# Kernel tuning notes

Hardware: AMD Instinct MI355X
Metric: run time of the kernel (lower is better)

Reference implementation:

```python
import jax, jax.numpy as jnp
import numpy as np

N, E, F, H, OUT = 50000, 500000, 128, 128, 768

def _lin(x, W, b):
    return x @ W + b

def _layernorm(x, g, b, eps=1e-5):
    mu = jnp.mean(x, axis=-1, keepdims=True)
    var = jnp.var(x, axis=-1, keepdims=True)
    return (x - mu) * jax.lax.rsqrt(var + eps) * g + b

def _edge_softmax(alpha, dst, n_nodes):
    # softmax over incoming edges per destination node, per channel
    amax = jax.ops.segment_max(alpha, dst, num_segments=n_nodes)
    ex = jnp.exp(alpha - amax[dst])
    denom = jax.ops.segment_sum(ex, dst, num_segments=n_nodes)
    return ex / denom[dst]

def setup_inputs() -> dict:
    key = jax.random.key(0)
    ks = jax.random.split(key, 24)
    def w(k, i, o):
        return (jax.random.normal(k, (i, o), jnp.float32) / np.float32(np.sqrt(i)))
    inp = {
        'kind': jax.random.normal(ks[0], (N, F), jnp.float32),
        'edge_h': jax.random.normal(ks[1], (E, F), jnp.float32),
        'src': jax.random.randint(ks[2], (E,), 0, N, jnp.int32),
        'dst': jax.random.randint(ks[3], (E,), 0, N, jnp.int32),
        'KW': w(ks[4], 2 * F, H), 'Kb': jnp.zeros((H,), jnp.float32),
        'VW': w(ks[5], 2 * F, H), 'Vb': jnp.zeros((H,), jnp.float32),
        'QW': w(ks[6], F, H), 'Qb': jnp.zeros((H,), jnp.float32),
        'WW': w(ks[7], F + H, H), 'Wb': jnp.zeros((H,), jnp.float32),
        'K2W': w(ks[8], 3 * F, H), 'K2b': jnp.zeros((H,), jnp.float32),
        'V2W': w(ks[9], 3 * F, H), 'V2b': jnp.zeros((H,), jnp.float32),
        'Q2W': w(ks[10], 2 * F, H), 'Q2b': jnp.zeros((H,), jnp.float32),
        'W2W': w(ks[11], 2 * F + H, OUT), 'W2b': jnp.zeros((OUT,), jnp.float32),
        'ln1_g': jnp.ones((H,), jnp.float32), 'ln1_b': jnp.zeros((H,), jnp.float32),
        'ln2_g': jnp.ones((OUT,), jnp.float32), 'ln2_b': jnp.zeros((OUT,), jnp.float32),
        'gate_w': w(ks[12], OUT, 1), 'gate_b': jnp.zeros((1,), jnp.float32),
    }
    return inp

def reference(kind, edge_h, src, dst, KW, Kb, VW, Vb, QW, Qb, WW, Wb,
              K2W, K2b, V2W, V2b, Q2W, Q2b, W2W, W2b,
              ln1_g, ln1_b, ln2_g, ln2_b, gate_w, gate_b):
    n_nodes = kind.shape[0]
    src_kind = kind[src]                               # [E,F] gather
    # --- layer 1 ---
    Q = _lin(kind, QW, Qb)                             # [N,H]
    ek_in = jnp.concatenate([src_kind, edge_h], axis=1)  # [E,2F]
    eK = _lin(ek_in, KW, Kb)                           # [E,H]
    eV = _lin(ek_in, VW, Vb)                           # [E,H]
    alpha = _edge_softmax(Q[dst] * eK, dst, n_nodes)   # [E,H]
    h_n = jax.ops.segment_sum(alpha * eV, dst, num_segments=n_nodes)  # [N,H]
    h = _layernorm(_lin(jnp.concatenate([h_n, kind], axis=1), WW, Wb), ln1_g, ln1_b)
    # --- layer 2 ---
    Q2 = _lin(jnp.concatenate([kind, h], axis=1), Q2W, Q2b)            # [N,H]
    ek2_in = jnp.concatenate([src_kind, edge_h, h[src]], axis=1)       # [E,3F]
    eK2 = _lin(ek2_in, K2W, K2b)
    eV2 = _lin(ek2_in, V2W, V2b)
    alpha2 = _edge_softmax(Q2[dst] * eK2, dst, n_nodes)
    h_n1 = jax.ops.segment_sum(alpha2 * eV2, dst, num_segments=n_nodes)
    h1 = _layernorm(_lin(jnp.concatenate([h_n1, h, kind], axis=1), W2W, W2b), ln2_g, ln2_b)  # [N,768]
    # --- global attention pooling (single graph) ---
    gate = jax.nn.softmax(_lin(h1, gate_w, gate_b), axis=0)  # [N,1]
    graph_vec = jnp.sum(gate * h1, axis=0, keepdims=True)    # [1,768]
    return graph_vec
```

## Files before the change

kernel.cpp:

```cpp
#include <hip/hip_runtime.h>

typedef float f32x4 __attribute__((ext_vector_type(4)));
typedef short bf16x8 __attribute__((ext_vector_type(8)));
typedef unsigned short ushort8 __attribute__((ext_vector_type(8)));

__device__ __forceinline__ float bf2f(unsigned short u) {
    return __uint_as_float(((unsigned int)u) << 16);
}
__device__ __forceinline__ unsigned short f2bf(float f) {
    unsigned int u = __float_as_uint(f);
    u += 0x7FFFu + ((u >> 16) & 1u);
    return (unsigned short)(u >> 16);
}
__device__ __forceinline__ float pld(const void* p, long i, bool isbf) {
    return isbf ? bf2f(((const unsigned short*)p)[i]) : ((const float*)p)[i];
}

#define ASYNC16(gp, lp)                                                        \
    __builtin_amdgcn_global_load_lds(                                          \
        (__attribute__((address_space(1))) unsigned int*)(gp),                 \
        (__attribute__((address_space(3))) unsigned int*)(lp), 16, 0, 0)

__global__ void probe_kernel(const unsigned int* __restrict__ w, int* __restrict__ flag) {
    if (threadIdx.x == 0 && blockIdx.x == 0)
        *flag = (w[0] == 0x3F803F80u) ? 1 : 0;
}

__global__ __launch_bounds__(256) void cvt_kernel(
    const void* __restrict__ src_, unsigned short* __restrict__ dst_,
    const int* __restrict__ flag, long n8)
{
    const bool isbf = (*flag != 0);
    long stride = (long)gridDim.x * blockDim.x;
    for (long i = (long)blockIdx.x * blockDim.x + threadIdx.x; i < n8; i += stride) {
        if (isbf) {
            ((ushort8*)dst_)[i] = ((const ushort8*)src_)[i];
        } else {
            const float4* s = (const float4*)src_ + i * 2;
            float4 a = s[0], b = s[1];
            ushort8 r;
            r[0] = f2bf(a.x); r[1] = f2bf(a.y); r[2] = f2bf(a.z); r[3] = f2bf(a.w);
            r[4] = f2bf(b.x); r[5] = f2bf(b.y); r[6] = f2bf(b.z); r[7] = f2bf(b.w);
            ((ushort8*)dst_)[i] = r;
        }
    }
}

template <int WM, int WN, bool CVTA = false>
__global__ __launch_bounds__(256) void gemm_kernel(
    const void* __restrict__ seg0v, const unsigned short* __restrict__ seg1,
    const unsigned short* __restrict__ seg2,
    const int* __restrict__ gi0, const int* __restrict__ gi1, const int* __restrict__ gi2,
    const int* __restrict__ aflag,
    const unsigned short* __restrict__ Bt, const float* __restrict__ bias,
    int M, int K, int Nout,
    float* __restrict__ outF, unsigned short* __restrict__ outB)
{
    constexpr int BM = WM * 64, BN = WN * 64;
    constexpr int AI = BM / 64;
    constexpr int BI = BN / 64;
    constexpr int PB = BN + 8;
    constexpr int STAGE = (BM + BN) * 32 * 2;
    constexpr int PANEL = 16 * PB * 4;
    constexpr int SH = STAGE > PANEL ? STAGE : PANEL;
    __shared__ __attribute__((aligned(16))) char shraw[SH];
    unsigned short* lA = (unsigned short*)shraw;
    unsigned short* lB = lA + BM * 32;

    const int tid  = threadIdx.x;
    const int wave = tid >> 6, lane = tid & 63;
    const int wm = wave / WN, wn = wave % WN;

    const int rsub = tid >> 2;
    const int csel = (tid & 3) ^ ((tid >> 3) & 3);

    const unsigned short* seg0 = (const unsigned short*)seg0v;
    const unsigned short* aptr0[AI];
    const unsigned short* aptr1[AI];
    const unsigned short* aptr2[AI];
    const char* arowc[AI];
    bool af32 = false;
    if constexpr (CVTA) {
        af32 = (*aflag == 0);
        const int rb = af32 ? 512 : 256;
#pragma unroll
        for (int i = 0; i < AI; ++i) {
            int gr = blockIdx.x * BM + rsub + 64 * i;
            if (gr >= M) gr = M - 1;
            arowc[i] = (const char*)seg0v + (long)(gi0 ? gi0[gr] : gr) * rb;
        }
    } else {
#pragma unroll
        for (int i = 0; i < AI; ++i) {
            int gr = blockIdx.x * BM + rsub + 64 * i;
            if (gr >= M) gr = M - 1;
            aptr0[i] = seg0 + (long)(gi0 ? gi0[gr] : gr) * 128;
            aptr1[i] = seg1 ? seg1 + (long)(gi1 ? gi1[gr] : gr) * 128 : aptr0[i];
            aptr2[i] = seg2 ? seg2 + (long)(gi2 ? gi2[gr] : gr) * 128 : aptr0[i];
        }
    }
    const unsigned short* bptr[BI];
#pragma unroll
    for (int i = 0; i < BI; ++i) {
        int bn = blockIdx.y * BN + rsub + 64 * i;
        bptr[i] = Bt + (long)bn * K;
    }

    f32x4 acc[4][4];
#pragma unroll
    for (int a = 0; a < 4; ++a)
#pragma unroll
        for (int b = 0; b < 4; ++b) acc[a][b] = (f32x4)(0.0f);

    const int q = lane >> 4, mrow = lane & 15;

    auto compute_tile = [&]() {
        bf16x8 af[4], bfv[4];
#pragma unroll
        for (int t = 0; t < 4; ++t) {
            int r = wm * 64 + t * 16 + mrow;
            af[t] = *(const bf16x8*)&lA[r * 32 + ((q ^ ((r >> 1) & 3)) * 8)];
        }
#pragma unroll
        for (int t = 0; t < 4; ++t) {
            int r = wn * 64 + t * 16 + mrow;
            bfv[t] = *(const bf16x8*)&lB[r * 32 + ((q ^ ((r >> 1) & 3)) * 8)];
        }
#pragma unroll
        for (int tm = 0; tm < 4; ++tm)
#pragma unroll
            for (int tn = 0; tn < 4; ++tn)
                acc[tm][tn] = __builtin_amdgcn_mfma_f32_16x16x32_bf16(af[tm], bfv[tn], acc[tm][tn], 0, 0, 0);
    };

    if constexpr (CVTA) {
        ushort8 pfr[AI][4];
#pragma unroll
        for (int i = 0; i < AI; ++i) {
#pragma unroll
            for (int ks = 0; ks < 4; ++ks) {
                const int eo = ks * 32 + csel * 8;
                if (af32) {
                    const float4* s = (const float4*)((const float*)arowc[i] + eo);
                    float4 a = s[0], b = s[1];
                    ushort8 r;
                    r[0] = f2bf(a.x); r[1] = f2bf(a.y); r[2] = f2bf(a.z); r[3] = f2bf(a.w);
                    r[4] = f2bf(b.x); r[5] = f2bf(b.y); r[6] = f2bf(b.z); r[7] = f2bf(b.w);
                    pfr[i][ks] = r;
                } else {
                    pfr[i][ks] = *(const ushort8*)((const unsigned short*)arowc[i] + eo);
                }
            }
        }
#pragma unroll
        for (int ks = 0; ks < 4; ++ks) {
            __syncthreads();
#pragma unroll
            for (int i = 0; i < AI; ++i)
                *(ushort8*)&lA[tid * 8 + i * 2048] = pfr[i][ks];
#pragma unroll
            for (int i = 0; i < BI; ++i)
                ASYNC16(bptr[i] + ks * 32 + csel * 8, &lB[tid * 8 + i * 2048]);
            __syncthreads();
            compute_tile();
        }
    } else {
        for (int kk = 0; kk < K; kk += 32) {
            __syncthreads();
            const int s = kk >> 7, koff = kk & 127;
#pragma unroll
            for (int i = 0; i < AI; ++i) {
                const unsigned short* ap = (s == 0) ? aptr0[i] : ((s == 1) ? aptr1[i] : aptr2[i]);
                ASYNC16(ap + koff + csel * 8, &lA[tid * 8 + i * 2048]);
            }
#pragma unroll
            for (int i = 0; i < BI; ++i) {
                ASYNC16(bptr[i] + kk + csel * 8, &lB[tid * 8 + i * 2048]);
            }
            __syncthreads();
            compute_tile();
        }
    }

    float bv[4];
#pragma unroll
    for (int tn = 0; tn < 4; ++tn) {
        int col = blockIdx.y * BN + wn * 64 + tn * 16 + mrow;
        bv[tn] = bias ? bias[col] : 0.0f;
    }
    float*          pf = (float*)shraw;
    unsigned short* pb = (unsigned short*)shraw;

#pragma unroll
    for (int p = 0; p < BM / 16; ++p) {
        const int pw = p >> 2;
        const int tm = p & 3;
        __syncthreads();
        if (wm == pw) {
#pragma unroll
            for (int tn = 0; tn < 4; ++tn) {
                int cl = wn * 64 + tn * 16 + mrow;
#pragma unroll
                for (int r = 0; r < 4; ++r) {
                    int pr = q * 4 + r;
                    float v = acc[tm][tn][r] + bv[tn];
                    if (outF) pf[pr * PB + cl] = v;
                    else      pb[pr * PB + cl] = f2bf(v);
                }
            }
        }
        __syncthreads();
        const int rowbase = blockIdx.x * BM + p * 16;
        if (outF) {
            constexpr int CPR = BN / 4;
            for (int c = tid; c < 16 * CPR; c += 256) {
                int pr = c / CPR, co = (c - pr * CPR) * 4;
                int grow = rowbase + pr;
                if (grow < M)
                    *(float4*)(outF + (long)grow * Nout + blockIdx.y * BN + co) =
                        *(const float4*)(pf + pr * PB + co);
            }
        } else {
            constexpr int CPR = BN / 8;
            for (int c = tid; c < 16 * CPR; c += 256) {
                int pr = c / CPR, co = (c - pr * CPR) * 8;
                int grow = rowbase + pr;
                if (grow < M)
                    *(ushort8*)(outB + (long)grow * Nout + blockIdx.y * BN + co) =
                        *(const ushort8*)(pb + pr * PB + co);
            }
        }
    }
}

__global__ void hist_kernel(const int* __restrict__ dst, int* __restrict__ counts, int E) {
    int e = blockIdx.x * blockDim.x + threadIdx.x;
    if (e < E) atomicAdd(&counts[dst[e]], 1);
}

__global__ __launch_bounds__(1024) void scan_kernel(const int* __restrict__ counts,
                                                    int* __restrict__ indptr,
                                                    int* __restrict__ wp, int N) {
    __shared__ int wsum[16];
    __shared__ int carry;
    int tid = threadIdx.x;
    int wave = tid >> 6, lane = tid & 63;
    if (tid == 0) carry = 0;
    __syncthreads();
    for (int base = 0; base < N; base += 1024) {
        int c0 = carry;
        int i = base + tid;
        int v = (i < N) ? counts[i] : 0;
        int s = v;
#pragma unroll
        for (int off = 1; off < 64; off <<= 1) {
            int t = __shfl_up(s, off, 64);
            if (lane >= off) s += t;
        }
        if (lane == 63) wsum[wave] = s;
        __syncthreads();
        if (wave == 0 && lane < 16) {
            int w = wsum[lane];
#pragma unroll
            for (int off = 1; off < 16; off <<= 1) {
                int t = __shfl_up(w, off, 64);
                if (lane >= off) w += t;
            }
            wsum[lane] = w;
        }
        __syncthreads();
        int woff = wave ? wsum[wave - 1] : 0;
        if (i < N) { int ex = c0 + woff + s - v; indptr[i] = ex; wp[i] = ex; }
        __syncthreads();
        if (tid == 0) carry = c0 + wsum[15];
        __syncthreads();
    }
    if (tid == 0) indptr[N] = carry;
}

__global__ void scatter_kernel(const int* __restrict__ dst, const int* __restrict__ src,
                               int* __restrict__ wp,
                               int* __restrict__ eidx, int* __restrict__ srcs, int E) {
    int e = blockIdx.x * blockDim.x + threadIdx.x;
    if (e < E) {
        int slot = atomicAdd(&wp[dst[e]], 1);
        eidx[slot] = e;
        srcs[slot] = src[e];
    }
}

__global__ __launch_bounds__(256) void edge_softmax_kernel(
    const int* __restrict__ indptr, const int* __restrict__ srcs,
    const float* __restrict__ Q, const unsigned short* __restrict__ ekv,
    const unsigned short* __restrict__ nkv,
    unsigned short* __restrict__ hn, int N, int off)
{
    int wave = threadIdx.x >> 6, lane = threadIdx.x & 63;
    int n = blockIdx.x * 4 + wave;
    if (n >= N) return;
    int beg = indptr[n], end = indptr[n + 1];
    int c = lane << 1;
    float q0 = Q[(long)n * 128 + c], q1 = Q[(long)n * 128 + c + 1];

    float mA0 = -3.4e38f, mA1 = -3.4e38f, dA0 = 0.f, dA1 = 0.f, aA0 = 0.f, aA1 = 0.f;
    float mB0 = -3.4e38f, mB1 = -3.4e38f, dB0 = 0.f, dB1 = 0.f, aB0 = 0.f, aB1 = 0.f;

    auto step = [&](int i, float& m0, float& m1, float& d0, float& d1,
                    float& a0, float& a1) {
        int sv = srcs[i];
        const unsigned short* er = ekv + (long)i * 512 + off + c;
        const unsigned short* nr = nkv + (long)sv * 256 + c;
        unsigned int kk = *(const unsigned int*)er;
        unsigned int vv = *(const unsigned int*)(er + 128);
        unsigned int nk = *(const unsigned int*)nr;
        unsigned int nv = *(const unsigned int*)(nr + 128);
        float k0 = bf2f((unsigned short)kk) + bf2f((unsigned short)nk);
        float k1 = bf2f((unsigned short)(kk >> 16)) + bf2f((unsigned short)(nk >> 16));
        float v0 = bf2f((unsigned short)vv) + bf2f((unsigned short)nv);
        float v1 = bf2f((unsigned short)(vv >> 16)) + bf2f((unsigned short)(nv >> 16));
        float s0 = q0 * k0, s1 = q1 * k1;
        float nm0 = fmaxf(m0, s0), nm1 = fmaxf(m1, s1);
        float e00 = __expf(m0 - nm0), e01 = __expf(s0 - nm0);
        float e10 = __expf(m1 - nm1), e11 = __expf(s1 - nm1);
        d0 = d0 * e00 + e01; a0 = a0 * e00 + e01 * v0; m0 = nm0;
        d1 = d1 * e10 + e11; a1 = a1 * e10 + e11 * v1; m1 = nm1;
    };

    int i = beg;
    for (; i + 2 <= end; i += 2) {
        step(i,     mA0, mA1, dA0, dA1, aA0, aA1);
        step(i + 1, mB0, mB1, dB0, dB1, aB0, aB1);
    }
    if (i < end) step(i, mA0, mA1, dA0, dA1, aA0, aA1);

    float M0 = fmaxf(mA0, mB0), M1 = fmaxf(mA1, mB1);
    float eA0 = __expf(mA0 - M0), eB0 = __expf(mB0 - M0);
    float eA1 = __expf(mA1 - M1), eB1 = __expf(mB1 - M1);
    float d0 = dA0 * eA0 + dB0 * eB0, a0 = aA0 * eA0 + aB0 * eB0;
    float d1 = dA1 * eA1 + dB1 * eB1, a1 = aA1 * eA1 + aB1 * eB1;

    float r0 = (end > beg) ? a0 / d0 : 0.f;
    float r1 = (end > beg) ? a1 / d1 : 0.f;
    unsigned int pk = (unsigned int)f2bf(r0) | ((unsigned int)f2bf(r1) << 16);
    *(unsigned int*)(hn + (long)n * 128 + c) = pk;
}

__global__ __launch_bounds__(256) void ln128_kernel(
    const float* __restrict__ x, const float* __restrict__ g,
    const float* __restrict__ b, unsigned short* __restrict__ y, int N)
{
    int wave = threadIdx.x >> 6, lane = threadIdx.x & 63;
    int n = blockIdx.x * 4 + wave;
    if (n >= N) return;
    int c = lane << 1;
    float2 v = *(const float2*)(x + (long)n * 128 + c);
    float s = v.x + v.y;
#pragma unroll
    for (int o = 1; o < 64; o <<= 1) s += __shfl_xor(s, o, 64);
    float mu = s * (1.f / 128.f);
    float dx0 = v.x - mu, dx1 = v.y - mu;
    float sq = dx0 * dx0 + dx1 * dx1;
#pragma unroll
    for (int o = 1; o < 64; o <<= 1) sq += __shfl_xor(sq, o, 64);
    float rs = rsqrtf(sq * (1.f / 128.f) + 1e-5f);
    float y0 = dx0 * rs * g[c] + b[c];
    float y1 = dx1 * rs * g[c + 1] + b[c + 1];
    unsigned int pk = (unsigned int)f2bf(y0) | ((unsigned int)f2bf(y1) << 16);
    *(unsigned int*)(y + (long)n * 128 + c) = pk;
}

__global__ __launch_bounds__(256) void ln768_kernel(
    const float* __restrict__ x, const float* __restrict__ g,
    const float* __restrict__ b, const float* __restrict__ gw,
    const float* __restrict__ gbias,
    unsigned short* __restrict__ y, float* __restrict__ gout, int N)
{
    __shared__ float red[4];
    __shared__ float red2[4];
    int n = blockIdx.x;
    int tid = threadIdx.x;
    int wave = tid >> 6, lane = tid & 63;
    const float* xr = x + (long)n * 768;
    float v0 = xr[tid], v1 = xr[tid + 256], v2 = xr[tid + 512];
    float s = v0 + v1 + v2;
#pragma unroll
    for (int o = 1; o < 64; o <<= 1) s += __shfl_xor(s, o, 64);
    if (lane == 0) red[wave] = s;
    __syncthreads();
    float mu = (red[0] + red[1] + red[2] + red[3]) * (1.f / 768.f);
    float d0 = v0 - mu, d1 = v1 - mu, d2 = v2 - mu;
    float sq = d0 * d0 + d1 * d1 + d2 * d2;
#pragma unroll
    for (int o = 1; o < 64; o <<= 1) sq += __shfl_xor(sq, o, 64);
    __syncthreads();
    if (lane == 0) red[wave] = sq;
    __syncthreads();
    float rs = rsqrtf((red[0] + red[1] + red[2] + red[3]) * (1.f / 768.f) + 1e-5f);
    float y0 = d0 * rs * g[tid]       + b[tid];
    float y1 = d1 * rs * g[tid + 256] + b[tid + 256];
    float y2 = d2 * rs * g[tid + 512] + b[tid + 512];
    unsigned short* yr = y + (long)n * 768;
    yr[tid]       = f2bf(y0);
    yr[tid + 256] = f2bf(y1);
    yr[tid + 512] = f2bf(y2);
    float dot = y0 * gw[tid] + y1 * gw[tid + 256] + y2 * gw[tid + 512];
#pragma unroll
    for (int o = 1; o < 64; o <<= 1) dot += __shfl_xor(dot, o, 64);
    if (lane == 0) red2[wave] = dot;
    __syncthreads();
    if (tid == 0) gout[n] = red2[0] + red2[1] + red2[2] + red2[3] + gbias[0];
}

__global__ __launch_bounds__(256) void reduce_max_kernel(
    const float* __restrict__ gv, unsigned int* __restrict__ gmax, int N)
{
    __shared__ float red[4];
    int tid = threadIdx.x, wave = tid >> 6, lane = tid & 63;
    float m = -3.4e38f;
    for (int i = blockIdx.x * 256 + tid; i < N; i += gridDim.x * 256)
        m = fmaxf(m, gv[i]);
#pragma unroll
    for (int o = 1; o < 64; o <<= 1) m = fmaxf(m, __shfl_xor(m, o, 64));
    if (lane == 0) red[wave] = m;
    __syncthreads();
    if (tid == 0) {
        m = fmaxf(fmaxf(red[0], red[1]), fmaxf(red[2], red[3]));
        unsigned int u = __float_as_uint(m);
        u = (u & 0x80000000u) ? ~u : (u | 0x80000000u);
        atomicMax(gmax, u);
    }
}

__global__ __launch_bounds__(256) void gate_acc_kernel(
    const unsigned short* __restrict__ h1, const float* __restrict__ gv,
    const unsigned int* __restrict__ gmax_u, float* __restrict__ num,
    float* __restrict__ Z, int N)
{
    unsigned int mu = *gmax_u;
    float gm = (mu & 0x80000000u) ? __uint_as_float(mu & 0x7FFFFFFFu) : __uint_as_float(~mu);
    int tid = threadIdx.x;
    float a0 = 0.f, a1 = 0.f, a2 = 0.f, z = 0.f;
    for (int n = blockIdx.x; n < N; n += gridDim.x) {
        float ex = __expf(gv[n] - gm);
        const unsigned short* hr = h1 + (long)n * 768;
        a0 += ex * bf2f(hr[tid]);
        a1 += ex * bf2f(hr[tid + 256]);
        a2 += ex * bf2f(hr[tid + 512]);
        z += ex;
    }
    atomicAdd(num + tid, a0);
    atomicAdd(num + tid + 256, a1);
    atomicAdd(num + tid + 512, a2);
    if (tid == 0) atomicAdd(Z, z);
}

__global__ void finalize_kernel(const float* __restrict__ num, const float* __restrict__ Z,
                                void* __restrict__ out, const int* __restrict__ flag) {
    int i = blockIdx.x * blockDim.x + threadIdx.x;
    if (i < 768) {
        float v = num[i] / *Z;
        if (*flag) ((unsigned short*)out)[i] = f2bf(v);
        else       ((float*)out)[i] = v;
    }
}

__global__ void transpose_kernel(
    const void* QW, const void* KW, const void* VW, const void* WW,
    const void* Q2W, const void* K2W, const void* V2W, const void* W2W,
    unsigned short* tQ, unsigned short* tNKV1, unsigned short* tEKV,
    unsigned short* tW, unsigned short* tQ2,
    unsigned short* tNKV2, unsigned short* tW2,
    const int* __restrict__ flag)
{
    const bool isbf = (*flag != 0);
    const int mode = blockIdx.y;
    unsigned short* dstp; int Kd, Nr;
    switch (mode) {
        case 0:  dstp = tQ;              Kd = 128; Nr = 128; break;
        case 1:  dstp = tNKV1;           Kd = 128; Nr = 256; break;
        case 2:  dstp = tEKV;            Kd = 128; Nr = 256; break;
        case 3:  dstp = tW;              Kd = 256; Nr = 128; break;
        case 4:  dstp = tQ2;             Kd = 256; Nr = 128; break;
        case 5:  dstp = tNKV2;           Kd = 256; Nr = 256; break;
        case 6:  dstp = tEKV + 256*128;  Kd = 128; Nr = 256; break;
        default: dstp = tW2;             Kd = 384; Nr = 768; break;
    }
    int total = Kd * Nr;
    for (int idx = blockIdx.x * blockDim.x + threadIdx.x; idx < total;
         idx += gridDim.x * blockDim.x) {
        int n = idx / Kd, k = idx - n * Kd;
        float v;
        switch (mode) {
            case 0:  v = pld(QW,  (long)k * 128 + n, isbf); break;
            case 1:  v = pld(n < 128 ? KW : VW, (long)k * 128 + (n & 127), isbf); break;
            case 2:  v = pld(n < 128 ? KW : VW, (long)(k + 128) * 128 + (n & 127), isbf); break;
            case 3:  v = pld(WW,  (long)k * 128 + n, isbf); break;
            case 4:  v = pld(Q2W, (long)k * 128 + n, isbf); break;
            case 5:  v = pld(n < 128 ? K2W : V2W,
                             (long)(k < 128 ? k : k + 128) * 128 + (n & 127), isbf); break;
            case 6:  v = pld(n < 128 ? K2W : V2W, (long)(k + 128) * 128 + (n & 127), isbf); break;
            default: v = pld(W2W, (long)k * 768 + n, isbf); break;
        }
        dstp[(long)n * Kd + k] = f2bf(v);
    }
}

__global__ void init_kernel(
    const int* __restrict__ flag, int* counts, float* num, float* Z, unsigned int* gmax,
    const void* Qb, const void* Kb, const void* Vb, const void* Wb,
    const void* Q2b, const void* K2b, const void* V2b, const void* W2b,
    const void* l1g, const void* l1b, const void* l2g, const void* l2b,
    const void* gw, const void* gb,
    float* bQ, float* bKV, float* bW, float* bQ2, float* bKV2, float* bW2,
    float* f1g, float* f1b, float* f2g, float* f2b, float* fgw, float* fgb, int N)
{
    const bool isbf = (*flag != 0);
    int i = blockIdx.x * blockDim.x + threadIdx.x;
    if (i < N) counts[i] = 0;
    if (i < 768) {
        num[i] = 0.f;
        bW2[i] = pld(W2b, i, isbf);
        f2g[i] = pld(l2g, i, isbf); f2b[i] = pld(l2b, i, isbf);
        fgw[i] = pld(gw, i, isbf);
    }
    if (i < 128) {
        bQ[i] = pld(Qb, i, isbf); bW[i] = pld(Wb, i, isbf); bQ2[i] = pld(Q2b, i, isbf);
        bKV[i] = pld(Kb, i, isbf);  bKV[i + 128] = pld(Vb, i, isbf);
        bKV2[i] = pld(K2b, i, isbf); bKV2[i + 128] = pld(V2b, i, isbf);
        f1g[i] = pld(l1g, i, isbf); f1b[i] = pld(l1b, i, isbf);
    }
    if (i == 0) { *Z = 0.f; *gmax = 0u; fgb[0] = pld(gb, 0, isbf); }
}

extern "C" void kernel_launch(void* const* d_in, const int* in_sizes, int n_in,
                              void* d_out, int out_size, void* d_ws, size_t ws_size,
                              hipStream_t stream)
{
    const void* kind   = d_in[0];
    const void* edge_h = d_in[1];
    const int* src = (const int*)d_in[2];
    const int* dst = (const int*)d_in[3];
    const void* KW  = d_in[4];  const void* Kb  = d_in[5];
    const void* VW  = d_in[6];  const void* Vb  = d_in[7];
    const void* QW  = d_in[8];  const void* Qb  = d_in[9];
    const void* WW  = d_in[10]; const void* Wb  = d_in[11];
    const void* K2W = d_in[12]; const void* K2b = d_in[13];
    const void* V2W = d_in[14]; const void* V2b = d_in[15];
    const void* Q2W = d_in[16]; const void* Q2b = d_in[17];
    const void* W2W = d_in[18]; const void* W2b = d_in[19];
    const void* ln1g = d_in[20]; const void* ln1b = d_in[21];
    const void* ln2g = d_in[22]; const void* ln2b = d_in[23];
    const void* gw  = d_in[24]; const void* gb  = d_in[25];

    const int N = in_sizes[0] / 128;
    const int E = in_sizes[2];

    char* wsp = (char*)d_ws;
    auto alloc = [&](size_t bytes) -> char* {
        char* p = wsp;
        wsp += (bytes + 255) & ~(size_t)255;
        return p;
    };
    unsigned short* tQ    = (unsigned short*)alloc(128 * 128 * 2);
    unsigned short* tNKV1 = (unsigned short*)alloc(256 * 128 * 2);
    unsigned short* tEKV  = (unsigned short*)alloc(512 * 128 * 2);
    unsigned short* tW    = (unsigned short*)alloc(128 * 256 * 2);
    unsigned short* tQ2   = (unsigned short*)alloc(128 * 256 * 2);
    unsigned short* tNKV2 = (unsigned short*)alloc(256 * 256 * 2);
    unsigned short* tW2   = (unsigned short*)alloc(768 * 384 * 2);
    float* bQ   = (float*)alloc(128 * 4);
    float* bKV  = (float*)alloc(256 * 4);
    float* bW   = (float*)alloc(128 * 4);
    float* bQ2  = (float*)alloc(128 * 4);
    float* bKV2 = (float*)alloc(256 * 4);
    float* bW2  = (float*)alloc(768 * 4);
    float* f1g = (float*)alloc(128 * 4);
    float* f1b = (float*)alloc(128 * 4);
    float* f2g = (float*)alloc(768 * 4);
    float* f2b = (float*)alloc(768 * 4);
    float* fgw = (float*)alloc(768 * 4);
    float* fgb = (float*)alloc(256);
    int*   flag = (int*)alloc(256);
    unsigned short* kindB = (unsigned short*)alloc((size_t)N * 128 * 2);
    float* Qbuf = (float*)alloc((size_t)N * 128 * 4);
    unsigned short* nkv1 = (unsigned short*)alloc((size_t)N * 256 * 2);
    unsigned short* nkv2 = (unsigned short*)alloc((size_t)N * 256 * 2);

    size_t h1off = ((size_t)N * 768 * 4 + 255) & ~(size_t)255;
    size_t bigsz = (size_t)E * 1024;
    size_t need  = h1off + (size_t)N * 768 * 2;
    if (need > bigsz) bigsz = need;
    char* big = alloc(bigsz);
    unsigned short* ekv   = (unsigned short*)big;
    float*          preh1 = (float*)big;
    unsigned short* h1    = (unsigned short*)(big + h1off);

    unsigned short* hn = (unsigned short*)alloc((size_t)N * 128 * 2);
    unsigned short* h  = (unsigned short*)alloc((size_t)N * 128 * 2);
    int* counts = (int*)alloc((size_t)N * 4);
    int* indptr = (int*)alloc((size_t)(N + 1) * 4);
    int* wp     = (int*)alloc((size_t)N * 4);
    int* eidx   = (int*)alloc((size_t)E * 4);
    int* srcs   = (int*)alloc((size_t)E * 4);
    float* g    = (float*)alloc((size_t)N * 4);
    unsigned int* gmaxp = (unsigned int*)alloc(256);
    float* Zp   = (float*)alloc(256);
    float* nump = (float*)alloc(768 * 4);

    probe_kernel<<<1, 64, 0, stream>>>((const unsigned int*)ln1g, flag);
    init_kernel<<<(N + 255) / 256, 256, 0, stream>>>(
        flag, counts, nump, Zp, gmaxp, Qb, Kb, Vb, Wb, Q2b, K2b, V2b, W2b,
        ln1g, ln1b, ln2g, ln2b, gw, gb,
        bQ, bKV, bW, bQ2, bKV2, bW2, f1g, f1b, f2g, f2b, fgw, fgb, N);
    transpose_kernel<<<dim3(64, 8), 256, 0, stream>>>(
        QW, KW, VW, WW, Q2W, K2W, V2W, W2W,
        tQ, tNKV1, tEKV, tW, tQ2, tNKV2, tW2, flag);
    cvt_kernel<<<512, 256, 0, stream>>>(kind, kindB, flag, (long)N * 16);
    hist_kernel<<<(E + 255) / 256, 256, 0, stream>>>(dst, counts, E);
    scan_kernel<<<1, 1024, 0, stream>>>(counts, indptr, wp, N);
    scatter_kernel<<<(E + 255) / 256, 256, 0, stream>>>(dst, src, wp, eidx, srcs, E);

    gemm_kernel<1, 4, true><<<dim3((E + 63) / 64, 2), 256, 0, stream>>>(
        edge_h, nullptr, nullptr, eidx, nullptr, nullptr, flag,
        tEKV, nullptr, E, 128, 512, nullptr, ekv);

    gemm_kernel<2, 2><<<dim3((N + 127) / 128, 1), 256, 0, stream>>>(
        kindB, nullptr, nullptr, nullptr, nullptr, nullptr, nullptr,
        tQ, bQ, N, 128, 128, Qbuf, nullptr);
    gemm_kernel<2, 2><<<dim3((N + 127) / 128, 2), 256, 0, stream>>>(
        kindB, nullptr, nullptr, nullptr, nullptr, nullptr, nullptr,
        tNKV1, bKV, N, 128, 256, nullptr, nkv1);
    edge_softmax_kernel<<<(N + 3) / 4, 256, 0, stream>>>(
        indptr, srcs, Qbuf, ekv, nkv1, hn, N, 0);
    gemm_kernel<2, 2><<<dim3((N + 127) / 128, 1), 256, 0, stream>>>(
        hn, kindB, nullptr, nullptr, nullptr, nullptr, nullptr,
        tW, bW, N, 256, 128, Qbuf, nullptr);
    ln128_kernel<<<(N + 3) / 4, 256, 0, stream>>>(Qbuf, f1g, f1b, h, N);

    gemm_kernel<2, 2><<<dim3((N + 127) / 128, 1), 256, 0, stream>>>(
        kindB, h, nullptr, nullptr, nullptr, nullptr, nullptr,
        tQ2, bQ2, N, 256, 128, Qbuf, nullptr);
    gemm_kernel<2, 2><<<dim3((N + 127) / 128, 2), 256, 0, stream>>>(
        kindB, h, nullptr, nullptr, nullptr, nullptr, nullptr,
        tNKV2, bKV2, N, 256, 256, nullptr, nkv2);
    edge_softmax_kernel<<<(N + 3) / 4, 256, 0, stream>>>(
        indptr, srcs, Qbuf, ekv, nkv2, hn, N, 256);
    gemm_kernel<1, 4><<<dim3((N + 63) / 64, 3), 256, 0, stream>>>(
        hn, h, kindB, nullptr, nullptr, nullptr, nullptr,
        tW2, bW2, N, 384, 768, preh1, nullptr);
    ln768_kernel<<<N, 256, 0, stream>>>(preh1, f2g, f2b, fgw, fgb, h1, g, N);

    reduce_max_kernel<<<256, 256, 0, stream>>>(g, gmaxp, N);
    gate_acc_kernel<<<256, 256, 0, stream>>>(h1, g, gmaxp, nump, Zp, N);
    finalize_kernel<<<3, 256, 0, stream>>>(nump, Zp, d_out, flag);
}
```

Before: 1.277 ms.

## Enlarge edge GEMM tile to 128x256 with 512 threads, widen softmax ILP

The GEMM kernel is generalized to thread counts of WM*WN*64, and the edge K/V projection now uses 128x256 tiles with 512 threads. This doubles reuse of each B tile and halves the grid size. The CVTA path no longer prefetches all four K-slices of A into registers up front; it loads and converts each slice just before its compute step, which cuts register pressure but removes that prefetch overlap. The edge softmax loop now keeps four independent online-softmax accumulators instead of two, giving the gather loads more memory-level parallelism at the cost of extra registers.

Result: faster. 1.224 ms (-4.2%).

```diff
diff --git a/kernel.cpp b/kernel.cpp
--- a/kernel.cpp
+++ b/kernel.cpp
@@ -47,7 +47,7 @@
 }
 
 template <int WM, int WN, bool CVTA = false>
-__global__ __launch_bounds__(256) void gemm_kernel(
+__global__ __launch_bounds__(WM * WN * 64) void gemm_kernel(
     const void* __restrict__ seg0v, const unsigned short* __restrict__ seg1,
     const unsigned short* __restrict__ seg2,
     const int* __restrict__ gi0, const int* __restrict__ gi1, const int* __restrict__ gi2,
@@ -56,9 +56,11 @@
     int M, int K, int Nout,
     float* __restrict__ outF, unsigned short* __restrict__ outB)
 {
+    constexpr int NT = WM * WN * 64;
     constexpr int BM = WM * 64, BN = WN * 64;
-    constexpr int AI = BM / 64;
-    constexpr int BI = BN / 64;
+    constexpr int RPC = NT / 4;
+    constexpr int AI = BM / RPC;
+    constexpr int BI = BN / RPC;
     constexpr int PB = BN + 8;
     constexpr int STAGE = (BM + BN) * 32 * 2;
     constexpr int PANEL = 16 * PB * 4;
@@ -85,14 +87,14 @@
         const int rb = af32 ? 512 : 256;
 #pragma unroll
         for (int i = 0; i < AI; ++i) {
-            int gr = blockIdx.x * BM + rsub + 64 * i;
+            int gr = blockIdx.x * BM + rsub + RPC * i;
             if (gr >= M) gr = M - 1;
             arowc[i] = (const char*)seg0v + (long)(gi0 ? gi0[gr] : gr) * rb;
         }
     } else {
 #pragma unroll
         for (int i = 0; i < AI; ++i) {
-            int gr = blockIdx.x * BM + rsub + 64 * i;
+            int gr = blockIdx.x * BM + rsub + RPC * i;
             if (gr >= M) gr = M - 1;
             aptr0[i] = seg0 + (long)(gi0 ? gi0[gr] : gr) * 128;
             aptr1[i] = seg1 ? seg1 + (long)(gi1 ? gi1[gr] : gr) * 128 : aptr0[i];
@@ -102,7 +104,7 @@
     const unsigned short* bptr[BI];
 #pragma unroll
     for (int i = 0; i < BI; ++i) {
-        int bn = blockIdx.y * BN + rsub + 64 * i;
+        int bn = blockIdx.y * BN + rsub + RPC * i;
         bptr[i] = Bt + (long)bn * K;
     }
 
@@ -134,33 +136,26 @@
     };
 
     if constexpr (CVTA) {
-        ushort8 pfr[AI][4];
-#pragma unroll
-        for (int i = 0; i < AI; ++i) {
-#pragma unroll
-            for (int ks = 0; ks < 4; ++ks) {
-                const int eo = ks * 32 + csel * 8;
+#pragma unroll
+        for (int ks = 0; ks < 4; ++ks) {
+            __syncthreads();
+#pragma unroll
+            for (int i = 0; i < BI; ++i)
+                ASYNC16(bptr[i] + ks * 32 + csel * 8, &lB[tid * 8 + i * NT * 8]);
+            const int eo = ks * 32 + csel * 8;
+#pragma unroll
+            for (int i = 0; i < AI; ++i) {
+                ushort8 r;
                 if (af32) {
                     const float4* s = (const float4*)((const float*)arowc[i] + eo);
                     float4 a = s[0], b = s[1];
-                    ushort8 r;
                     r[0] = f2bf(a.x); r[1] = f2bf(a.y); r[2] = f2bf(a.z); r[3] = f2bf(a.w);
                     r[4] = f2bf(b.x); r[5] = f2bf(b.y); r[6] = f2bf(b.z); r[7] = f2bf(b.w);
-                    pfr[i][ks] = r;
                 } else {
-                    pfr[i][ks] = *(const ushort8*)((const unsigned short*)arowc[i] + eo);
+                    r = *(const ushort8*)((const unsigned short*)arowc[i] + eo);
                 }
+                *(ushort8*)&lA[tid * 8 + i * NT * 8] = r;
             }
-        }
-#pragma unroll
-        for (int ks = 0; ks < 4; ++ks) {
-            __syncthreads();
-#pragma unroll
-            for (int i = 0; i < AI; ++i)
-                *(ushort8*)&lA[tid * 8 + i * 2048] = pfr[i][ks];
-#pragma unroll
-            for (int i = 0; i < BI; ++i)
-                ASYNC16(bptr[i] + ks * 32 + csel * 8, &lB[tid * 8 + i * 2048]);
             __syncthreads();
             compute_tile();
         }
@@ -171,11 +166,11 @@
 #pragma unroll
             for (int i = 0; i < AI; ++i) {
                 const unsigned short* ap = (s == 0) ? aptr0[i] : ((s == 1) ? aptr1[i] : aptr2[i]);
-                ASYNC16(ap + koff + csel * 8, &lA[tid * 8 + i * 2048]);
+                ASYNC16(ap + koff + csel * 8, &lA[tid * 8 + i * NT * 8]);
             }
 #pragma unroll
             for (int i = 0; i < BI; ++i) {
-                ASYNC16(bptr[i] + kk + csel * 8, &lB[tid * 8 + i * 2048]);
+                ASYNC16(bptr[i] + kk + csel * 8, &lB[tid * 8 + i * NT * 8]);
             }
             __syncthreads();
             compute_tile();
@@ -213,7 +208,7 @@
         const int rowbase = blockIdx.x * BM + p * 16;
         if (outF) {
             constexpr int CPR = BN / 4;
-            for (int c = tid; c < 16 * CPR; c += 256) {
+            for (int c = tid; c < 16 * CPR; c += NT) {
                 int pr = c / CPR, co = (c - pr * CPR) * 4;
                 int grow = rowbase + pr;
                 if (grow < M)
@@ -222,7 +217,7 @@
             }
         } else {
             constexpr int CPR = BN / 8;
-            for (int c = tid; c < 16 * CPR; c += 256) {
+            for (int c = tid; c < 16 * CPR; c += NT) {
                 int pr = c / CPR, co = (c - pr * CPR) * 8;
                 int grow = rowbase + pr;
                 if (grow < M)
@@ -302,11 +297,14 @@
     int c = lane << 1;
     float q0 = Q[(long)n * 128 + c], q1 = Q[(long)n * 128 + c + 1];
 
-    float mA0 = -3.4e38f, mA1 = -3.4e38f, dA0 = 0.f, dA1 = 0.f, aA0 = 0.f, aA1 = 0.f;
-    float mB0 = -3.4e38f, mB1 = -3.4e38f, dB0 = 0.f, dB1 = 0.f, aB0 = 0.f, aB1 = 0.f;
-
-    auto step = [&](int i, float& m0, float& m1, float& d0, float& d1,
-                    float& a0, float& a1) {
+    float m0[4], m1[4], dv0[4], dv1[4], av0[4], av1[4];
+#pragma unroll
+    for (int j = 0; j < 4; ++j) {
+        m0[j] = -3.4e38f; m1[j] = -3.4e38f;
+        dv0[j] = 0.f; dv1[j] = 0.f; av0[j] = 0.f; av1[j] = 0.f;
+    }
+
+    auto step = [&](int i, int j) {
         int sv = srcs[i];
         const unsigned short* er = ekv + (long)i * 512 + off + c;
         const unsigned short* nr = nkv + (long)sv * 256 + c;
@@ -319,25 +317,28 @@
         float v0 = bf2f((unsigned short)vv) + bf2f((unsigned short)nv);
         float v1 = bf2f((unsigned short)(vv >> 16)) + bf2f((unsigned short)(nv >> 16));
         float s0 = q0 * k0, s1 = q1 * k1;
-        float nm0 = fmaxf(m0, s0), nm1 = fmaxf(m1, s1);
-        float e00 = __expf(m0 - nm0), e01 = __expf(s0 - nm0);
-        float e10 = __expf(m1 - nm1), e11 = __expf(s1 - nm1);
-        d0 = d0 * e00 + e01; a0 = a0 * e00 + e01 * v0; m0 = nm0;
-        d1 = d1 * e10 + e11; a1 = a1 * e10 + e11 * v1; m1 = nm1;
+        float nm0 = fmaxf(m0[j], s0), nm1 = fmaxf(m1[j], s1);
+        float e00 = __expf(m0[j] - nm0), e01 = __expf(s0 - nm0);
+        float e10 = __expf(m1[j] - nm1), e11 = __expf(s1 - nm1);
+        dv0[j] = dv0[j] * e00 + e01; av0[j] = av0[j] * e00 + e01 * v0; m0[j] = nm0;
+        dv1[j] = dv1[j] * e10 + e11; av1[j] = av1[j] * e10 + e11 * v1; m1[j] = nm1;
     };
 
     int i = beg;
-    for (; i + 2 <= end; i += 2) {
-        step(i,     mA0, mA1, dA0, dA1, aA0, aA1);
-        step(i + 1, mB0, mB1, dB0, dB1, aB0, aB1);
-    }
-    if (i < end) step(i, mA0, mA1, dA0, dA1, aA0, aA1);
-
-    float M0 = fmaxf(mA0, mB0), M1 = fmaxf(mA1, mB1);
-    float eA0 = __expf(mA0 - M0), eB0 = __expf(mB0 - M0);
-    float eA1 = __expf(mA1 - M1), eB1 = __expf(mB1 - M1);
-    float d0 = dA0 * eA0 + dB0 * eB0, a0 = aA0 * eA0 + aB0 * eB0;
-    float d1 = dA1 * eA1 + dB1 * eB1, a1 = aA1 * eA1 + aB1 * eB1;
+    for (; i + 4 <= end; i += 4) {
+        step(i, 0); step(i + 1, 1); step(i + 2, 2); step(i + 3, 3);
+    }
+    for (; i < end; ++i) step(i, 0);
+
+    float M0 = fmaxf(fmaxf(m0[0], m0[1]), fmaxf(m0[2], m0[3]));
+    float M1 = fmaxf(fmaxf(m1[0], m1[1]), fmaxf(m1[2], m1[3]));
+    float d0 = 0.f, a0 = 0.f, d1 = 0.f, a1 = 0.f;
+#pragma unroll
+    for (int j = 0; j < 4; ++j) {
+        float e0 = __expf(m0[j] - M0), e1 = __expf(m1[j] - M1);
+        d0 += dv0[j] * e0; a0 += av0[j] * e0;
+        d1 += dv1[j] * e1; a1 += av1[j] * e1;
+    }
 
     float r0 = (end > beg) ? a0 / d0 : 0.f;
     float r1 = (end > beg) ? a1 / d1 : 0.f;
@@ -620,7 +621,7 @@
     scan_kernel<<<1, 1024, 0, stream>>>(counts, indptr, wp, N);
     scatter_kernel<<<(E + 255) / 256, 256, 0, stream>>>(dst, src, wp, eidx, srcs, E);
 
-    gemm_kernel<1, 4, true><<<dim3((E + 63) / 64, 2), 256, 0, stream>>>(
+    gemm_kernel<2, 4, true><<<dim3((E + 127) / 128, 2), 512, 0, stream>>>(
         edge_h, nullptr, nullptr, eidx, nullptr, nullptr, flag,
         tEKV, nullptr, E, 128, 512, nullptr, ekv);
 
```
